# Optimization experiments

Measured on AMD Instinct MI355X. Metric: run time of the kernel, lower is better.

Reference implementation:

```python
import jax, jax.numpy as jnp
import numpy as np

B, N, K, H, C = 16, 2048, 9, 128, 2  # K = nb_neighbors, kernel_size = K+1


def setup_inputs() -> dict:
    key = jax.random.key(0)
    ks = jax.random.split(key, 7)
    s = 0.1
    x = jax.random.normal(ks[0], (B, N, C), jnp.float32)
    Wconv = jax.random.normal(ks[1], (H, C, K + 1), jnp.float32) * s  # conv1d weight
    bconv = jax.random.normal(ks[2], (H,), jnp.float32) * s
    W1 = jax.random.normal(ks[3], (H, C), jnp.float32) * s
    b1 = jax.random.normal(ks[4], (H,), jnp.float32) * s
    W2 = jax.random.normal(ks[5], (H, H), jnp.float32) * s
    b2 = jax.random.normal(ks[6], (H,), jnp.float32) * s
    return {"x": x, "Wconv": Wconv, "bconv": bconv, "W1": W1, "b1": b1, "W2": W2, "b2": b2}


def reference(x, Wconv, bconv, W1, b1, W2, b2):
    # node embedding: W1(x)
    node_emb = jnp.einsum('bnc,hc->bnh', x, W1) + b1  # (B,N,H)

    # pairwise Euclidean distances (B,N,N) via the GEMM form
    sq = jnp.sum(x * x, axis=-1)  # (B,N)
    d2 = sq[:, :, None] + sq[:, None, :] - 2.0 * jnp.einsum('bnc,bmc->bnm', x, x)
    dist = jnp.sqrt(jnp.maximum(d2, 0.0))

    # torch: topk(k=N) (descending) then take last K+1 columns -> the K+1
    # smallest distances ordered descending (nearest/self last)
    knn = jnp.flip(jnp.argsort(dist, axis=-1)[..., : K + 1], axis=-1)  # (B,N,K+1)

    # batched gather of neighbor coords: (B,N,K+1,C)
    coords = jax.vmap(lambda xb, ib: xb[ib])(x, knn)

    # conv1d with kernel spanning the full window -> single output position,
    # i.e. a contraction over (channel, position)
    conv_emb = jnp.einsum('bnkc,hck->bnh', coords, Wconv) + bconv  # (B,N,H)
    conv_emb = jnp.einsum('bnh,eh->bne', conv_emb, W2) + b2

    return node_emb + conv_emb
```

## Files before the change

kernel.cpp:

```cpp
#include <hip/hip_runtime.h>
#include <cfloat>
#include <stdint.h>

#define B_   16
#define N_   2048
#define KK   10
#define H_   128
#define SUB  32
#define NCH  (N_ / SUB)

#define RANK_BLOCKS (B_ * 16)
#define WEFF_ELEMS  (H_ * KK * 2 + H_)
#define WEFF_BLOCKS ((WEFF_ELEMS + 63) / 64)

__device__ inline uint32_t f32_ordered(float f) {
    uint32_t u = __float_as_uint(f);
    return (u & 0x80000000u) ? ~u : (u | 0x80000000u);
}

__global__ __launch_bounds__(64) void setup_kernel(
    const float* __restrict__ x,
    const float* __restrict__ Wconv, const float* __restrict__ bconv,
    const float* __restrict__ b1,    const float* __restrict__ W2,
    const float* __restrict__ b2,
    float4* __restrict__ xsorted,
    float*  __restrict__ weff,
    float*  __restrict__ btot)
{
#pragma clang fp contract(off)
    __shared__ __align__(16) uint64_t sk[N_];
    const int tid = threadIdx.x;

    if (blockIdx.x >= RANK_BLOCKS) {
        int gid = (blockIdx.x - RANK_BLOCKS) * 64 + tid;
        if (gid < H_ * KK * 2) {
            int e = gid / 20, r = gid % 20, k = r >> 1, c = r & 1;
            float acc = 0.f;
#pragma unroll 8
            for (int h = 0; h < H_; ++h)
                acc += W2[e * H_ + h] * Wconv[h * (2 * KK) + c * KK + k];
            weff[gid] = acc;
        } else if (gid < H_ * KK * 2 + H_) {
            int e = gid - H_ * KK * 2;
            float acc = b1[e] + b2[e];
#pragma unroll 8
            for (int h = 0; h < H_; ++h) acc += W2[e * H_ + h] * bconv[h];
            btot[e] = acc;
        }
        return;
    }

    const int b   = blockIdx.x >> 4;
    const int seg = blockIdx.x & 15;
    const float2* xb = (const float2*)(x + (size_t)b * N_ * 2);

    for (int i = tid; i < N_; i += 64)
        sk[i] = ((uint64_t)f32_ordered(xb[i].x) << 32) | (uint32_t)i;
    __syncthreads();

    const int i0 = seg * 128 + tid;
    const int i1 = i0 + 64;
    const uint64_t k0 = sk[i0];
    const uint64_t k1 = sk[i1];
    int r0 = 0, r1 = 0;
    const ulonglong2* sk2 = (const ulonglong2*)sk;
#pragma unroll 8
    for (int j = 0; j < N_ / 2; ++j) {
        ulonglong2 kk = sk2[j];
        r0 += (int)(kk.x < k0) + (int)(kk.y < k0);
        r1 += (int)(kk.x < k1) + (int)(kk.y < k1);
    }

    float2 p0 = xb[i0];
    float2 p1 = xb[i1];
    float sm0 = p0.x * p0.x + p0.y * p0.y;
    float sm1 = p1.x * p1.x + p1.y * p1.y;
    xsorted[(size_t)b * N_ + r0] =
        make_float4(p0.x, p0.y, sm0, __uint_as_float((uint32_t)i0));
    xsorted[(size_t)b * N_ + r1] =
        make_float4(p1.x, p1.y, sm1, __uint_as_float((uint32_t)i1));
}

__global__ __launch_bounds__(512, 4) void knn_conv_kernel(
    const float4* __restrict__ xsorted,
    const float* __restrict__ W1,
    const float* __restrict__ weff,
    const float* __restrict__ btot,
    float* __restrict__ out)
{
#pragma clang fp contract(off)
    __shared__ float4   xs4[N_];
    __shared__ uint64_t mkeys[64 * 81];
    __shared__ float    wcoord[64 * 21];
    __shared__ float    hbound[8 * 64];

    const int tid  = threadIdx.x;
    const int w    = tid >> 6;
    const int l    = tid & 63;
    const int b    = blockIdx.x >> 5;
    const int tile = blockIdx.x & 31;

    const float4* xb = xsorted + (size_t)b * N_;
    for (int i = tid; i < N_; i += 512) xs4[i] = xb[i];
    __syncthreads();

    const int    n  = tile * 64 + l;
    const float4 qv = xs4[n];
    const float  qx = qv.x, qy = qv.y, sqn = qv.z;
    const float  qa  = xs4[tile * 64].x;
    const float  qbx = xs4[tile * 64 + 63].x;

    const uint64_t KINIT = (((uint64_t)0x7F7FFFFFu) << 32) | 0x3FFFFFu;
    uint64_t hk[KK];
#pragma unroll
    for (int j = 0; j < KK; ++j) hk[j] = KINIT;
    float h9d  = FLT_MAX;
    float shb  = FLT_MAX;
    float gate = FLT_MAX;

    auto scan_chunk = [&](int mc) {
        for (int mm = 0; mm < SUB; ++mm) {
            const int m = mc + mm;
            float4 c4 = xs4[m];
            float s  = sqn + c4.z;
            float pr = qx * c4.x;
            float dt = __builtin_fmaf(qy, c4.y, pr);
            float d2 = __builtin_fmaf(-2.0f, dt, s);
            float dc = d2 > 0.0f ? d2 : 0.0f;
            if (dc <= gate) {
                uint32_t oi = __float_as_uint(c4.w);
                uint64_t key = ((uint64_t)__float_as_uint(dc) << 32)
                             | (oi << 11) | (uint32_t)m;
                if (key < hk[KK - 1]) {
#pragma unroll
                    for (int j = KK - 1; j >= 1; --j) {
                        bool cj  = key < hk[j];
                        bool cjm = key < hk[j - 1];
                        hk[j] = cj ? (cjm ? hk[j - 1] : key) : hk[j];
                    }
                    hk[0] = (key < hk[0]) ? key : hk[0];
                }
                h9d  = __uint_as_float((uint32_t)(hk[KK - 1] >> 32));
                gate = fminf(h9d, shb);
            }
        }
    };

    const int ct2 = 2 * tile;
    const int a   = (w - ct2) & 7;
    const int c1  = ct2 + a;
    const int c2  = c1 - 8;
    int c_near = (a <= 4) ? c1 : c2;
    if (c1 > NCH - 1) c_near = c2;
    if (c2 < 0)       c_near = c1;
    scan_chunk(c_near * SUB);

    hbound[w * 64 + l] = h9d;
    __syncthreads();
    {
        float m0 = fminf(hbound[0 * 64 + l], hbound[1 * 64 + l]);
        float m1 = fminf(hbound[2 * 64 + l], hbound[3 * 64 + l]);
        float m2 = fminf(hbound[4 * 64 + l], hbound[5 * 64 + l]);
        float m3 = fminf(hbound[6 * 64 + l], hbound[7 * 64 + l]);
        shb  = fminf(fminf(m0, m1), fminf(m2, m3));
        gate = fminf(h9d, shb);
    }

    int  cl = c_near - 8, cr = c_near + 8;
    bool la = (cl >= 0), ra = (cr <= NCH - 1);
    while (la || ra) {
        float wm = gate;
        wm = fmaxf(wm, __shfl_xor(wm, 1,  64));
        wm = fmaxf(wm, __shfl_xor(wm, 2,  64));
        wm = fmaxf(wm, __shfl_xor(wm, 4,  64));
        wm = fmaxf(wm, __shfl_xor(wm, 8,  64));
        wm = fmaxf(wm, __shfl_xor(wm, 16, 64));
        wm = fmaxf(wm, __shfl_xor(wm, 32, 64));
        float gl = la ? (qa - xs4[cl * SUB + SUB - 1].x) : FLT_MAX;
        float gr = ra ? (xs4[cr * SUB].x - qbx)          : FLT_MAX;
        bool pickL = la && (!ra || gl <= gr);
        if (pickL) {
            if (__builtin_fmaf(gl, gl, -4e-6f) > wm) la = false;
            else { scan_chunk(cl * SUB); cl -= 8; la = (cl >= 0); }
        } else {
            if (__builtin_fmaf(gr, gr, -4e-6f) > wm) ra = false;
            else { scan_chunk(cr * SUB); cr += 8; ra = (cr <= NCH - 1); }
        }
    }

    {
        const int mb = l * 81 + w * 10;
#pragma unroll
        for (int j = 0; j < KK; ++j) mkeys[mb + j] = hk[j];
    }

    const int e = tid & 127;
    float we[20];
    {
        const float4* wp = (const float4*)(weff + e * 20);
#pragma unroll
        for (int r = 0; r < 5; ++r) {
            float4 v = wp[r];
            we[4 * r + 0] = v.x; we[4 * r + 1] = v.y;
            we[4 * r + 2] = v.z; we[4 * r + 3] = v.w;
        }
    }
    const float w1x = W1[e * 2 + 0];
    const float w1y = W1[e * 2 + 1];
    const float bt  = btot[e];
    __syncthreads();

    {
        const int q = tid >> 3;
        const int r = tid & 7;
        const int mb = q * 81 + r * 10;
        int p = 0;
#pragma unroll
        for (int sel = 0; sel < KK; ++sel) {
            uint64_t v = (p < KK) ? mkeys[mb + p] : 0xFFFFFFFFFFFFFFFFull;
            uint64_t t1 = __shfl_xor((unsigned long long)v, 1, 64);
            uint64_t m1 = v  < t1 ? v  : t1;
            uint64_t t2 = __shfl_xor((unsigned long long)m1, 2, 64);
            uint64_t m2 = m1 < t2 ? m1 : t2;
            uint64_t t4 = __shfl_xor((unsigned long long)m2, 4, 64);
            uint64_t vm = m2 < t4 ? m2 : t4;
            if (v == vm) {
                ++p;
                float4 c = xs4[(int)(vm & 0x7FF)];
                const int k = (KK - 1) - sel;
                wcoord[q * 21 + 2 * k + 0] = c.x;
                wcoord[q * 21 + 2 * k + 1] = c.y;
            }
        }
    }
    __syncthreads();

    const int qb_ = tid >> 7;
    const size_t obase = (size_t)b * N_ * H_;
#pragma unroll
    for (int jj = 0; jj < 16; ++jj) {
        const int qq = qb_ + 4 * jj;
        float4 xq = xs4[tile * 64 + qq];
        uint32_t orig = __float_as_uint(xq.w);
        const float* wc = &wcoord[qq * 21];
        float acc = bt;
        acc += xq.x * w1x;
        acc += xq.y * w1y;
#pragma unroll
        for (int k = 0; k < KK; ++k) {
            acc += wc[2 * k + 0] * we[2 * k + 0];
            acc += wc[2 * k + 1] * we[2 * k + 1];
        }
        out[obase + (size_t)orig * H_ + e] = acc;
    }
}

extern "C" void kernel_launch(void* const* d_in, const int* in_sizes, int n_in,
                              void* d_out, int out_size, void* d_ws, size_t ws_size,
                              hipStream_t stream) {
    const float* x     = (const float*)d_in[0];
    const float* Wconv = (const float*)d_in[1];
    const float* bconv = (const float*)d_in[2];
    const float* W1    = (const float*)d_in[3];
    const float* b1    = (const float*)d_in[4];
    const float* W2    = (const float*)d_in[5];
    const float* b2    = (const float*)d_in[6];
    float* out  = (float*)d_out;
    float* weff = (float*)d_ws;
    float* btot = weff + H_ * KK * 2;
    float4* xsorted = (float4*)((char*)d_ws + 16384);

    setup_kernel<<<dim3(RANK_BLOCKS + WEFF_BLOCKS), dim3(64), 0, stream>>>(
        x, Wconv, bconv, b1, W2, b2, xsorted, weff, btot);
    knn_conv_kernel<<<dim3(B_ * (N_ / 64)), dim3(512), 0, stream>>>(
        xsorted, W1, weff, btot, out);
}
```

Before: 177.5 us.

## Widen setup kernel parallelism and batch distance loads in KNN scan

The rank-sort setup now uses 256-thread blocks with twice as many blocks. Each element's rank is counted by four partial-range threads and then summed through shared memory, so the serial 2048-compare loop per thread becomes 512 compares. The weight-folding path splits each dot product across four lanes and combines them with shuffles. The KNN scan loads four candidates and computes their distances before the gated inserts, to expose more ILP. The cost is extra shared memory and a sync in setup, and possibly higher register pressure in the scan.

```diff
diff --git a/kernel.cpp b/kernel.cpp
--- a/kernel.cpp
+++ b/kernel.cpp
@@ -9,16 +9,16 @@
 #define SUB  32
 #define NCH  (N_ / SUB)
 
-#define RANK_BLOCKS (B_ * 16)
-#define WEFF_ELEMS  (H_ * KK * 2 + H_)
-#define WEFF_BLOCKS ((WEFF_ELEMS + 63) / 64)
+#define RANK_BLOCKS (B_ * 32)
+#define WEFF_OUT    (H_ * KK * 2 + H_)
+#define WEFF_BLOCKS ((WEFF_OUT * 4) / 256)
 
 __device__ inline uint32_t f32_ordered(float f) {
     uint32_t u = __float_as_uint(f);
     return (u & 0x80000000u) ? ~u : (u | 0x80000000u);
 }
 
-__global__ __launch_bounds__(64) void setup_kernel(
+__global__ __launch_bounds__(256) void setup_kernel(
     const float* __restrict__ x,
     const float* __restrict__ Wconv, const float* __restrict__ bconv,
     const float* __restrict__ b1,    const float* __restrict__ W2,
@@ -29,56 +29,74 @@
 {
 #pragma clang fp contract(off)
     __shared__ __align__(16) uint64_t sk[N_];
+    __shared__ int pcnt[4 * 64];
     const int tid = threadIdx.x;
 
     if (blockIdx.x >= RANK_BLOCKS) {
-        int gid = (blockIdx.x - RANK_BLOCKS) * 64 + tid;
-        if (gid < H_ * KK * 2) {
-            int e = gid / 20, r = gid % 20, k = r >> 1, c = r & 1;
-            float acc = 0.f;
+        const int g = (blockIdx.x - RANK_BLOCKS) * 256 + tid;
+        const int o = g >> 2, q = g & 3;
+        float acc = 0.f;
+        if (o < H_ * KK * 2) {
+            const int e = o / 20, r = o % 20, k = r >> 1, c = r & 1;
+            const float* w2p = W2 + e * H_ + q * 32;
+            const float* wcp = Wconv + (q * 32) * (2 * KK) + c * KK + k;
 #pragma unroll 8
-            for (int h = 0; h < H_; ++h)
-                acc += W2[e * H_ + h] * Wconv[h * (2 * KK) + c * KK + k];
-            weff[gid] = acc;
-        } else if (gid < H_ * KK * 2 + H_) {
-            int e = gid - H_ * KK * 2;
-            float acc = b1[e] + b2[e];
+            for (int h = 0; h < 32; ++h)
+                acc += w2p[h] * wcp[h * (2 * KK)];
+        } else {
+            const int e = o - H_ * KK * 2;
+            const float* w2p = W2 + e * H_ + q * 32;
+            const float* bcp = bconv + q * 32;
 #pragma unroll 8
-            for (int h = 0; h < H_; ++h) acc += W2[e * H_ + h] * bconv[h];
-            btot[e] = acc;
+            for (int h = 0; h < 32; ++h) acc += w2p[h] * bcp[h];
+        }
+        acc += __shfl_xor(acc, 1, 64);
+        acc += __shfl_xor(acc, 2, 64);
+        if (q == 0) {
+            if (o < H_ * KK * 2) weff[o] = acc;
+            else {
+                const int e = o - H_ * KK * 2;
+                btot[e] = acc + b1[e] + b2[e];
+            }
         }
         return;
     }
 
-    const int b   = blockIdx.x >> 4;
-    const int seg = blockIdx.x & 15;
+    const int b  = blockIdx.x >> 5;
+    const int sg = blockIdx.x & 31;
     const float2* xb = (const float2*)(x + (size_t)b * N_ * 2);
 
-    for (int i = tid; i < N_; i += 64)
+    for (int i = tid; i < N_; i += 256)
         sk[i] = ((uint64_t)f32_ordered(xb[i].x) << 32) | (uint32_t)i;
     __syncthreads();
 
-    const int i0 = seg * 128 + tid;
-    const int i1 = i0 + 64;
-    const uint64_t k0 = sk[i0];
-    const uint64_t k1 = sk[i1];
-    int r0 = 0, r1 = 0;
-    const ulonglong2* sk2 = (const ulonglong2*)sk;
-#pragma unroll 8
-    for (int j = 0; j < N_ / 2; ++j) {
-        ulonglong2 kk = sk2[j];
-        r0 += (int)(kk.x < k0) + (int)(kk.y < k0);
-        r1 += (int)(kk.x < k1) + (int)(kk.y < k1);
-    }
-
-    float2 p0 = xb[i0];
-    float2 p1 = xb[i1];
-    float sm0 = p0.x * p0.x + p0.y * p0.y;
-    float sm1 = p1.x * p1.x + p1.y * p1.y;
-    xsorted[(size_t)b * N_ + r0] =
-        make_float4(p0.x, p0.y, sm0, __uint_as_float((uint32_t)i0));
-    xsorted[(size_t)b * N_ + r1] =
-        make_float4(p1.x, p1.y, sm1, __uint_as_float((uint32_t)i1));
+    const int el = tid & 63;
+    const int pt = tid >> 6;
+    const uint64_t kown = sk[sg * 64 + el];
+    const ulonglong2* sk2 = (const ulonglong2*)sk + pt * 256;
+    int cnt = 0;
+#pragma unroll 2
+    for (int j = 0; j < 256; j += 4) {
+        ulonglong2 t0 = sk2[j + 0];
+        ulonglong2 t1 = sk2[j + 1];
+        ulonglong2 t2 = sk2[j + 2];
+        ulonglong2 t3 = sk2[j + 3];
+        cnt += (int)(t0.x < kown) + (int)(t0.y < kown)
+             + (int)(t1.x < kown) + (int)(t1.y < kown)
+             + (int)(t2.x < kown) + (int)(t2.y < kown)
+             + (int)(t3.x < kown) + (int)(t3.y < kown);
+    }
+    pcnt[pt * 64 + el] = cnt;
+    __syncthreads();
+
+    if (tid < 64) {
+        const int r = pcnt[tid] + pcnt[64 + tid] + pcnt[128 + tid] + pcnt[192 + tid];
+        const int i = sg * 64 + tid;
+        float2 p = xb[i];
+        float sm = p.x * p.x + p.y * p.y;
+        xsorted[(size_t)b * N_ + r] =
+            make_float4(p.x, p.y, sm, __uint_as_float((uint32_t)i));
+    }
 }
 
 __global__ __launch_bounds__(512, 4) void knn_conv_kernel(
@@ -118,41 +136,57 @@
     float shb  = FLT_MAX;
     float gate = FLT_MAX;
 
+    auto insert = [&](float dc, float cw, int m) {
+        uint32_t oi = __float_as_uint(cw);
+        uint64_t key = ((uint64_t)__float_as_uint(dc) << 32)
+                     | (oi << 11) | (uint32_t)m;
+        if (key < hk[KK - 1]) {
+#pragma unroll
+            for (int j = KK - 1; j >= 1; --j) {
+                bool cj  = key < hk[j];
+                bool cjm = key < hk[j - 1];
+                hk[j] = cj ? (cjm ? hk[j - 1] : key) : hk[j];
+            }
+            hk[0] = (key < hk[0]) ? key : hk[0];
+        }
+        h9d  = __uint_as_float((uint32_t)(hk[KK - 1] >> 32));
+        gate = fminf(h9d, shb);
+    };
+
     auto scan_chunk = [&](int mc) {
-        for (int mm = 0; mm < SUB; ++mm) {
-            const int m = mc + mm;
-            float4 c4 = xs4[m];
-            float s  = sqn + c4.z;
-            float pr = qx * c4.x;
-            float dt = __builtin_fmaf(qy, c4.y, pr);
-            float d2 = __builtin_fmaf(-2.0f, dt, s);
-            float dc = d2 > 0.0f ? d2 : 0.0f;
-            if (dc <= gate) {
-                uint32_t oi = __float_as_uint(c4.w);
-                uint64_t key = ((uint64_t)__float_as_uint(dc) << 32)
-                             | (oi << 11) | (uint32_t)m;
-                if (key < hk[KK - 1]) {
-#pragma unroll
-                    for (int j = KK - 1; j >= 1; --j) {
-                        bool cj  = key < hk[j];
-                        bool cjm = key < hk[j - 1];
-                        hk[j] = cj ? (cjm ? hk[j - 1] : key) : hk[j];
-                    }
-                    hk[0] = (key < hk[0]) ? key : hk[0];
-                }
-                h9d  = __uint_as_float((uint32_t)(hk[KK - 1] >> 32));
-                gate = fminf(h9d, shb);
-            }
+        for (int mm = 0; mm < SUB; mm += 4) {
+            const int m0 = mc + mm;
+            float4 c0 = xs4[m0 + 0];
+            float4 c1 = xs4[m0 + 1];
+            float4 c2 = xs4[m0 + 2];
+            float4 c3 = xs4[m0 + 3];
+            float dc0, dc1, dc2, dc3;
+            { float s = sqn + c0.z; float pr = qx * c0.x;
+              float dt = __builtin_fmaf(qy, c0.y, pr);
+              float d2 = __builtin_fmaf(-2.0f, dt, s); dc0 = d2 > 0.0f ? d2 : 0.0f; }
+            { float s = sqn + c1.z; float pr = qx * c1.x;
+              float dt = __builtin_fmaf(qy, c1.y, pr);
+              float d2 = __builtin_fmaf(-2.0f, dt, s); dc1 = d2 > 0.0f ? d2 : 0.0f; }
+            { float s = sqn + c2.z; float pr = qx * c2.x;
+              float dt = __builtin_fmaf(qy, c2.y, pr);
+              float d2 = __builtin_fmaf(-2.0f, dt, s); dc2 = d2 > 0.0f ? d2 : 0.0f; }
+            { float s = sqn + c3.z; float pr = qx * c3.x;
+              float dt = __builtin_fmaf(qy, c3.y, pr);
+              float d2 = __builtin_fmaf(-2.0f, dt, s); dc3 = d2 > 0.0f ? d2 : 0.0f; }
+            if (dc0 <= gate) insert(dc0, c0.w, m0 + 0);
+            if (dc1 <= gate) insert(dc1, c1.w, m0 + 1);
+            if (dc2 <= gate) insert(dc2, c2.w, m0 + 2);
+            if (dc3 <= gate) insert(dc3, c3.w, m0 + 3);
         }
     };
 
     const int ct2 = 2 * tile;
     const int a   = (w - ct2) & 7;
-    const int c1  = ct2 + a;
-    const int c2  = c1 - 8;
-    int c_near = (a <= 4) ? c1 : c2;
-    if (c1 > NCH - 1) c_near = c2;
-    if (c2 < 0)       c_near = c1;
+    const int c1_ = ct2 + a;
+    const int c2_ = c1_ - 8;
+    int c_near = (a <= 4) ? c1_ : c2_;
+    if (c1_ > NCH - 1) c_near = c2_;
+    if (c2_ < 0)       c_near = c1_;
     scan_chunk(c_near * SUB);
 
     hbound[w * 64 + l] = h9d;
@@ -270,7 +304,7 @@
     float* btot = weff + H_ * KK * 2;
     float4* xsorted = (float4*)((char*)d_ws + 16384);
 
-    setup_kernel<<<dim3(RANK_BLOCKS + WEFF_BLOCKS), dim3(64), 0, stream>>>(
+    setup_kernel<<<dim3(RANK_BLOCKS + WEFF_BLOCKS), dim3(256), 0, stream>>>(
         x, Wconv, bconv, b1, W2, b2, xsorted, weff, btot);
     knn_conv_kernel<<<dim3(B_ * (N_ / 64)), dim3(512), 0, stream>>>(
         xsorted, W1, weff, btot, out);
```

New measurement: 143.0 us. 1.24x faster.
